# Performance work log

Measured on AMD Instinct MI355X. Metric: run time of the kernel, lower is better.

Reference implementation:

```python
import jax, jax.numpy as jnp
import numpy as np

D_MODEL, H, D_FF = 1024, 16, 4096
D_K = D_MODEL // H
EPS = 1e-5


def _layernorm(x, alpha, bias):
    # faithful to source: unbiased std (ddof=1), eps added to std (not var)
    mean = jnp.mean(x, axis=-1, keepdims=True)
    std = jnp.std(x, axis=-1, keepdims=True, ddof=1)
    return alpha * (x - mean) / (std + EPS) + bias


def setup_inputs() -> dict:
    key = jax.random.key(0)
    ks = jax.random.split(key, 12)
    B, S = 2, 2048
    s = 1.0 / np.sqrt(D_MODEL)
    inp = {
        "x": jax.random.normal(ks[0], (B, S, D_MODEL), dtype=jnp.float32),
        "mask": jnp.ones((B, 1, 1, S), dtype=jnp.int32),
        "wq": jax.random.normal(ks[1], (D_MODEL, D_MODEL), dtype=jnp.float32) * s,
        "wk": jax.random.normal(ks[2], (D_MODEL, D_MODEL), dtype=jnp.float32) * s,
        "wv": jax.random.normal(ks[3], (D_MODEL, D_MODEL), dtype=jnp.float32) * s,
        "wo": jax.random.normal(ks[4], (D_MODEL, D_MODEL), dtype=jnp.float32) * s,
        "w1": jax.random.normal(ks[5], (D_MODEL, D_FF), dtype=jnp.float32) * s,
        "b1": jnp.zeros((D_FF,), dtype=jnp.float32),
        "w2": jax.random.normal(ks[6], (D_FF, D_MODEL), dtype=jnp.float32) * (1.0 / np.sqrt(D_FF)),
        "b2": jnp.zeros((D_MODEL,), dtype=jnp.float32),
        "alpha1": jnp.ones((1,), dtype=jnp.float32),
        "bias1": jnp.zeros((1,), dtype=jnp.float32),
        "alpha2": jnp.ones((1,), dtype=jnp.float32),
        "bias2": jnp.zeros((1,), dtype=jnp.float32),
    }
    return inp


def reference(x, mask, wq, wk, wv, wo, w1, b1, w2, b2, alpha1, bias1, alpha2, bias2):
    B, S, _ = x.shape

    # --- sublayer 1: pre-norm self-attention + residual ---
    xn = _layernorm(x, alpha1, bias1)
    q = (xn @ wq).reshape(B, S, H, D_K).transpose(0, 2, 1, 3)  # [B,H,S,Dk]
    k = (xn @ wk).reshape(B, S, H, D_K).transpose(0, 2, 1, 3)
    v = (xn @ wv).reshape(B, S, H, D_K).transpose(0, 2, 1, 3)

    scores = jnp.einsum("bhqd,bhkd->bhqk", q, k) / np.sqrt(D_K)  # [B,H,S,S]
    scores = jnp.where(mask == 0, jnp.float32(-1e9), scores)
    attn = jax.nn.softmax(scores, axis=-1)
    ctx = jnp.einsum("bhqk,bhkd->bhqd", attn, v)
    ctx = ctx.transpose(0, 2, 1, 3).reshape(B, S, D_MODEL)
    x = x + ctx @ wo

    # --- sublayer 2: pre-norm FFN + residual ---
    xn = _layernorm(x, alpha2, bias2)
    h = jax.nn.relu(xn @ w1 + b1)
    x = x + h @ w2 + b2
    return x
```

## Files before the change

kernel.cpp:

```cpp
#include <hip/hip_runtime.h>
#include <hip/hip_bf16.h>

typedef __attribute__((ext_vector_type(8))) short bf16x8;
typedef __attribute__((ext_vector_type(4))) short short4v;
typedef __attribute__((ext_vector_type(4))) float floatx4;

#define MFMA16(A, B, C) __builtin_amdgcn_mfma_f32_16x16x32_bf16((A), (B), (C), 0, 0, 0)

__device__ inline short bf16bits(float f) {
  __hip_bfloat16 h = __float2bfloat16(f);
  return *reinterpret_cast<short*>(&h);
}
__device__ inline unsigned cvtpk(float lo, float hi) {
  unsigned r;
  asm("v_cvt_pk_bf16_f32 %0, %1, %2" : "=v"(r) : "v"(lo), "v"(hi));
  return r;
}
typedef __attribute__((address_space(3))) char lds_char;
typedef __attribute__((address_space(1))) const char glob_char;
__device__ inline void gll16(const void* g, void* l) {
  __builtin_amdgcn_global_load_lds((glob_char*)g, (lds_char*)l, 16, 0, 0);
}

__global__ __launch_bounds__(256) void ln_qkvtrans_kernel(
    const float* __restrict__ x, __hip_bfloat16* __restrict__ y,
    const float* __restrict__ alpha_p, const float* __restrict__ bias_p,
    const float* __restrict__ wq, const float* __restrict__ wk,
    const float* __restrict__ wv, __hip_bfloat16* __restrict__ wqkvT) {
  __shared__ __align__(16) __hip_bfloat16 tile[64][72];
  const int bid = blockIdx.x;
  const int t = threadIdx.x;
  if (bid < 4096) {
    __shared__ float sred[8];
    const float* xr = x + (long)bid * 1024;
    float v[4];
#pragma unroll
    for (int i = 0; i < 4; i++) v[i] = xr[t * 4 + i];
    float sum = 0.f, sq = 0.f;
#pragma unroll
    for (int i = 0; i < 4; i++) { sum += v[i]; sq += v[i] * v[i]; }
#pragma unroll
    for (int off = 32; off; off >>= 1) {
      sum += __shfl_down(sum, off);
      sq += __shfl_down(sq, off);
    }
    if ((t & 63) == 0) { sred[(t >> 6) * 2] = sum; sred[(t >> 6) * 2 + 1] = sq; }
    __syncthreads();
    sum = sred[0] + sred[2] + sred[4] + sred[6];
    sq = sred[1] + sred[3] + sred[5] + sred[7];
    const float mean = sum * (1.f / 1024.f);
    float var = (sq - 1024.f * mean * mean) * (1.f / 1023.f);
    var = fmaxf(var, 0.f);
    const float denom = sqrtf(var) + 1e-5f;
    const float sc = alpha_p[0] / denom;
    const float beta = bias_p[0];
    __hip_bfloat16* yr = y + (long)bid * 1024;
#pragma unroll
    for (int i = 0; i < 4; i++) yr[t * 4 + i] = __float2bfloat16((v[i] - mean) * sc + beta);
  } else {
    const int tt = bid - 4096;
    const int which = tt >> 8;
    const float* src = which == 0 ? wq : (which == 1 ? wk : wv);
    __hip_bfloat16* dst = wqkvT + (size_t)which * 1024 * 1024;
    const long r0 = (long)((tt >> 4) & 15) * 64, c0 = (long)(tt & 15) * 64;
    for (int i = t; i < 1024; i += 256) {
      int r = i >> 4, c4 = (i & 15) * 4;
      float4 f = *(const float4*)&src[(r0 + r) * 1024 + c0 + c4];
      short4v s;
      s[0] = bf16bits(f.x); s[1] = bf16bits(f.y);
      s[2] = bf16bits(f.z); s[3] = bf16bits(f.w);
      *(short4v*)&tile[r][c4] = s;
    }
    __syncthreads();
    for (int i = t; i < 512; i += 256) {
      int c = i >> 3, r8 = (i & 7) * 8;
      bf16x8 sv;
#pragma unroll
      for (int j = 0; j < 8; j++) sv[j] = *reinterpret_cast<const short*>(&tile[r8 + j][c]);
      *(bf16x8*)&dst[(c0 + c) * 1024 + r0 + r8] = sv;
    }
  }
}

__global__ __launch_bounds__(256) void prep_kernel(
    const __hip_bfloat16* __restrict__ qkv, __hip_bfloat16* __restrict__ vt,
    const float* __restrict__ wo, __hip_bfloat16* __restrict__ woT,
    const int* __restrict__ mask, float* __restrict__ addm,
    int* __restrict__ flags) {
  __shared__ __align__(16) __hip_bfloat16 tile[64][72];
  __shared__ int ok[4];
  const int bid = blockIdx.x;
  if (bid < 1024) {
    const int bh = bid >> 5, b = bh >> 4, h = bh & 15;
    const long s0 = (long)(bid & 31) * 64;
    const __hip_bfloat16* src = qkv + ((long)b * 2048 + s0) * 3072 + 2048 + h * 64;
    for (int i = threadIdx.x; i < 512; i += 256) {
      int s = i >> 3, d8 = (i & 7) * 8;
      *(uint4*)&tile[s][d8] = *(const uint4*)&src[(long)s * 3072 + d8];
    }
    __syncthreads();
    __hip_bfloat16* dstb = vt + (long)bh * 64 * 2048 + s0;
    for (int i = threadIdx.x; i < 512; i += 256) {
      int d = i >> 3, s8 = (i & 7) * 8;
      bf16x8 sv;
#pragma unroll
      for (int j = 0; j < 8; j++) sv[j] = *reinterpret_cast<const short*>(&tile[s8 + j][d]);
      *(bf16x8*)&dstb[(long)d * 2048 + s8] = sv;
    }
  } else if (bid < 1280) {
    const int t = bid - 1024;
    const long r0 = (long)(t >> 4) * 64, c0 = (long)(t & 15) * 64;
    for (int i = threadIdx.x; i < 1024; i += 256) {
      int r = i >> 4, c4 = (i & 15) * 4;
      float4 f = *(const float4*)&wo[(r0 + r) * 1024 + c0 + c4];
      short4v s;
      s[0] = bf16bits(f.x); s[1] = bf16bits(f.y);
      s[2] = bf16bits(f.z); s[3] = bf16bits(f.w);
      *(short4v*)&tile[r][c4] = s;
    }
    __syncthreads();
    for (int i = threadIdx.x; i < 512; i += 256) {
      int c = i >> 3, r8 = (i & 7) * 8;
      bf16x8 sv;
#pragma unroll
      for (int j = 0; j < 8; j++) sv[j] = *reinterpret_cast<const short*>(&tile[r8 + j][c]);
      *(bf16x8*)&woT[(c0 + c) * 1024 + r0 + r8] = sv;
    }
  } else {
    const int i = (bid - 1280) * 256 + threadIdx.x;
    const int mv = mask[i];
    addm[i] = mv ? 0.f : -1e30f;
    const unsigned long long bal = __ballot(mv != 0);
    if ((threadIdx.x & 63) == 0) ok[threadIdx.x >> 6] = (bal == ~0ull) ? 1 : 0;
    __syncthreads();
    if (threadIdx.x == 0) flags[bid - 1280] = ok[0] & ok[1] & ok[2] & ok[3];
  }
}

__global__ __launch_bounds__(256) void wtrans_kernel(
    const float* __restrict__ w1c, const float* __restrict__ w2c,
    __hip_bfloat16* __restrict__ w1Th, __hip_bfloat16* __restrict__ w2Th) {
  __shared__ __align__(16) __hip_bfloat16 tile[64][72];
  const int bid = blockIdx.x;
  const float* src;
  __hip_bfloat16* dst;
  int R, ldS;
  long r0, c0;
  if (bid < 512) {
    src = w1c; dst = w1Th; R = 1024; ldS = 4096;
    r0 = (long)(bid >> 5) * 64; c0 = (long)(bid & 31) * 64;
  } else {
    const int t = bid - 512;
    src = w2c; dst = w2Th; R = 2048; ldS = 1024;
    r0 = (long)(t >> 4) * 64; c0 = (long)(t & 15) * 64;
  }
  for (int i = threadIdx.x; i < 1024; i += 256) {
    int r = i >> 4, c4 = (i & 15) * 4;
    float4 f = *(const float4*)&src[(r0 + r) * ldS + c0 + c4];
    short4v s;
    s[0] = bf16bits(f.x); s[1] = bf16bits(f.y);
    s[2] = bf16bits(f.z); s[3] = bf16bits(f.w);
    *(short4v*)&tile[r][c4] = s;
  }
  __syncthreads();
  for (int i = threadIdx.x; i < 512; i += 256) {
    int c = i >> 3, r8 = (i & 7) * 8;
    bf16x8 sv;
#pragma unroll
    for (int j = 0; j < 8; j++) sv[j] = *reinterpret_cast<const short*>(&tile[r8 + j][c]);
    *(bf16x8*)&dst[(c0 + c) * R + r0 + r8] = sv;
  }
}

__global__ __launch_bounds__(256) void bias_add_kernel(
    const float* __restrict__ x1, const float* __restrict__ b2,
    float* __restrict__ out) {
  const int i = (blockIdx.x * 256 + threadIdx.x) * 4;
  float4 v = *(const float4*)&x1[i];
  const float4 bb = *(const float4*)&b2[i & 1023];
  v.x += bb.x; v.y += bb.y; v.z += bb.z; v.w += bb.w;
  *(float4*)&out[i] = v;
}

__global__ __launch_bounds__(256) void ln_kernel(
    const float* __restrict__ x, __hip_bfloat16* __restrict__ y,
    const float* __restrict__ alpha_p, const float* __restrict__ bias_p) {
  __shared__ float sred[8];
  const long row = blockIdx.x;
  const int t = threadIdx.x;
  const float* xr = x + row * 1024;
  float v[4];
#pragma unroll
  for (int i = 0; i < 4; i++) v[i] = xr[t * 4 + i];
  float sum = 0.f, sq = 0.f;
#pragma unroll
  for (int i = 0; i < 4; i++) { sum += v[i]; sq += v[i] * v[i]; }
#pragma unroll
  for (int off = 32; off; off >>= 1) {
    sum += __shfl_down(sum, off);
    sq += __shfl_down(sq, off);
  }
  if ((t & 63) == 0) { sred[(t >> 6) * 2] = sum; sred[(t >> 6) * 2 + 1] = sq; }
  __syncthreads();
  sum = sred[0] + sred[2] + sred[4] + sred[6];
  sq = sred[1] + sred[3] + sred[5] + sred[7];
  const float mean = sum * (1.f / 1024.f);
  float var = (sq - 1024.f * mean * mean) * (1.f / 1023.f);
  var = fmaxf(var, 0.f);
  const float denom = sqrtf(var) + 1e-5f;
  const float sc = alpha_p[0] / denom;
  const float beta = bias_p[0];
  __hip_bfloat16* yr = y + row * 1024;
#pragma unroll
  for (int i = 0; i < 4; i++) yr[t * 4 + i] = __float2bfloat16((v[i] - mean) * sc + beta);
}

template <int EPI>
__global__ __launch_bounds__(256) void gemm_bt_kernel(
    const __hip_bfloat16* __restrict__ A, const __hip_bfloat16* __restrict__ Bt,
    void* __restrict__ Cv, const float* __restrict__ bias,
    const float* __restrict__ res, int M, int N, int K) {
  __shared__ __align__(16) __hip_bfloat16 lA[2][128 * 32];
  __shared__ __align__(16) __hip_bfloat16 lB[2][128 * 32];
  const int tid = threadIdx.x;
  const int wave = tid >> 6, lane = tid & 63;
  const int quad = lane >> 4, l16 = lane & 15;
  const int wm = wave >> 1, wn = wave & 1;

  const int gx = gridDim.x;
  const int nwg = gx * gridDim.y;
  int bid = blockIdx.y * gx + blockIdx.x;
  bid = (bid & 7) * (nwg >> 3) + (bid >> 3);
  const long m0 = (long)(bid / gx) * 128;
  const long n0 = (long)(bid % gx) * 128;

  const int rA0 = tid >> 2, cA0 = (tid & 3) * 8;
  const int rA1 = (tid + 256) >> 2, cA1 = ((tid + 256) & 3) * 8;

  floatx4 acc[4][4];
#pragma unroll
  for (int i = 0; i < 4; i++)
#pragma unroll
    for (int j = 0; j < 4; j++) acc[i][j] = (floatx4){0.f, 0.f, 0.f, 0.f};

  const __hip_bfloat16* Ab = A + m0 * K;
  const __hip_bfloat16* Bb = Bt + n0 * K;

  gll16(&Ab[(long)rA0 * K + cA0], &lA[0][wave * 512]);
  gll16(&Ab[(long)rA1 * K + cA1], &lA[0][2048 + wave * 512]);
  gll16(&Bb[(long)rA0 * K + cA0], &lB[0][wave * 512]);
  gll16(&Bb[(long)rA1 * K + cA1], &lB[0][2048 + wave * 512]);

  int cur = 0;
  for (int k0 = 0; k0 < K; k0 += 32) {
    __syncthreads();
    if (k0 + 32 < K) {
      const int nxt = cur ^ 1;
      gll16(&Ab[(long)rA0 * K + k0 + 32 + cA0], &lA[nxt][wave * 512]);
      gll16(&Ab[(long)rA1 * K + k0 + 32 + cA1], &lA[nxt][2048 + wave * 512]);
      gll16(&Bb[(long)rA0 * K + k0 + 32 + cA0], &lB[nxt][wave * 512]);
      gll16(&Bb[(long)rA1 * K + k0 + 32 + cA1], &lB[nxt][2048 + wave * 512]);
    }
    bf16x8 af[4], bfr[4];
#pragma unroll
    for (int mi = 0; mi < 4; mi++)
      af[mi] = *(const bf16x8*)&lA[cur][(wm * 64 + mi * 16 + l16) * 32 + quad * 8];
#pragma unroll
    for (int ni = 0; ni < 4; ni++)
      bfr[ni] = *(const bf16x8*)&lB[cur][(wn * 64 + ni * 16 + l16) * 32 + quad * 8];
#pragma unroll
    for (int mi = 0; mi < 4; mi++)
#pragma unroll
      for (int ni = 0; ni < 4; ni++)
        acc[mi][ni] = MFMA16(af[mi], bfr[ni], acc[mi][ni]);
    cur ^= 1;
  }

#pragma unroll
  for (int mi = 0; mi < 4; mi++) {
#pragma unroll
    for (int ni = 0; ni < 4; ni++) {
#pragma unroll
      for (int r = 0; r < 4; r++) {
        const long row = m0 + wm * 64 + mi * 16 + quad * 4 + r;
        const long col = n0 + wn * 64 + ni * 16 + l16;
        const long idx = row * N + col;
        float v = acc[mi][ni][r];
        if (EPI == 0) {
          ((__hip_bfloat16*)Cv)[idx] = __float2bfloat16(v);
        } else if (EPI == 1) {
          ((float*)Cv)[idx] = v + res[idx];
        } else if (EPI == 2) {
          v += bias[col];
          ((__hip_bfloat16*)Cv)[idx] = __float2bfloat16(fmaxf(v, 0.f));
        } else if (EPI == 3) {
          float* Cf = (float*)Cv;
          Cf[idx] = Cf[idx] + v;
        }
      }
    }
  }
}

template <int EPI>
__global__ __launch_bounds__(256) void gemm_bt_k64_kernel(
    const __hip_bfloat16* __restrict__ A, const __hip_bfloat16* __restrict__ Bt,
    void* __restrict__ Cv, const float* __restrict__ bias,
    const float* __restrict__ res, int M, int N, int K) {
  __shared__ __align__(16) __hip_bfloat16 lA[2][128 * 64];
  __shared__ __align__(16) __hip_bfloat16 lB[2][128 * 64];
  const int tid = threadIdx.x;
  const int wave = tid >> 6, lane = tid & 63;
  const int quad = lane >> 4, l16 = lane & 15;
  const int wm = wave >> 1, wn = wave & 1;

  const int gx = gridDim.x;
  const int nwg = gx * gridDim.y;
  int bid = blockIdx.y * gx + blockIdx.x;
  bid = (bid & 7) * (nwg >> 3) + (bid >> 3);
  const long m0 = (long)(bid / gx) * 128;
  const long n0 = (long)(bid % gx) * 128;

  const int srow = lane >> 3;
  const int cg = (lane & 7) ^ srow;

  floatx4 acc[4][4];
#pragma unroll
  for (int i = 0; i < 4; i++)
#pragma unroll
    for (int j = 0; j < 4; j++) acc[i][j] = (floatx4){0.f, 0.f, 0.f, 0.f};

  const __hip_bfloat16* Ab = A + m0 * K;
  const __hip_bfloat16* Bb = Bt + n0 * K;

#pragma unroll
  for (int j = 0; j < 4; ++j) {
    const int c = wave + j * 4;
    gll16(&Ab[(long)(c * 8 + srow) * K + cg * 8], &lA[0][c * 512]);
    gll16(&Bb[(long)(c * 8 + srow) * K + cg * 8], &lB[0][c * 512]);
  }

  int cur = 0;
  for (int k0 = 0; k0 < K; k0 += 64) {
    __syncthreads();
    if (k0 + 64 < K) {
      const int nxt = cur ^ 1;
#pragma unroll
      for (int j = 0; j < 4; ++j) {
        const int c = wave + j * 4;
        gll16(&Ab[(long)(c * 8 + srow) * K + k0 + 64 + cg * 8], &lA[nxt][c * 512]);
        gll16(&Bb[(long)(c * 8 + srow) * K + k0 + 64 + cg * 8], &lB[nxt][c * 512]);
      }
    }
#pragma unroll
    for (int ks = 0; ks < 2; ++ks) {
      bf16x8 af[4], bfr[4];
#pragma unroll
      for (int mi = 0; mi < 4; mi++) {
        const int row = wm * 64 + mi * 16 + l16;
        af[mi] = *(const bf16x8*)&lA[cur][row * 64 +
                                          (((ks * 4 + quad) ^ (l16 & 7)) * 8)];
      }
#pragma unroll
      for (int ni = 0; ni < 4; ni++) {
        const int row = wn * 64 + ni * 16 + l16;
        bfr[ni] = *(const bf16x8*)&lB[cur][row * 64 +
                                           (((ks * 4 + quad) ^ (l16 & 7)) * 8)];
      }
#pragma unroll
      for (int mi = 0; mi < 4; mi++)
#pragma unroll
        for (int ni = 0; ni < 4; ni++)
          acc[mi][ni] = MFMA16(af[mi], bfr[ni], acc[mi][ni]);
    }
    cur ^= 1;
  }

#pragma unroll
  for (int mi = 0; mi < 4; mi++) {
#pragma unroll
    for (int ni = 0; ni < 4; ni++) {
#pragma unroll
      for (int r = 0; r < 4; r++) {
        const long row = m0 + wm * 64 + mi * 16 + quad * 4 + r;
        const long col = n0 + wn * 64 + ni * 16 + l16;
        const long idx = row * N + col;
        float v = acc[mi][ni][r];
        if (EPI == 0) {
          ((__hip_bfloat16*)Cv)[idx] = __float2bfloat16(v);
        } else if (EPI == 1) {
          ((float*)Cv)[idx] = v + res[idx];
        } else if (EPI == 2) {
          v += bias[col];
          ((__hip_bfloat16*)Cv)[idx] = __float2bfloat16(fmaxf(v, 0.f));
        } else if (EPI == 3) {
          float* Cf = (float*)Cv;
          Cf[idx] = Cf[idx] + v;
        }
      }
    }
  }
}

template <int EPI>
__global__ __launch_bounds__(256) void gemm64_bt_kernel(
    const __hip_bfloat16* __restrict__ A, const __hip_bfloat16* __restrict__ Bt,
    void* __restrict__ Cv, const float* __restrict__ bias,
    const float* __restrict__ res, int M, int N, int K) {
  __shared__ __align__(16) __hip_bfloat16 lA[2][128 * 64];
  __shared__ __align__(16) __hip_bfloat16 lB[2][64 * 64];
  const int tid = threadIdx.x;
  const int wave = tid >> 6, lane = tid & 63;
  const int quad = lane >> 4, l16 = lane & 15;
  const int wm = wave >> 1, wn = wave & 1;

  const int gx = gridDim.x;
  const int nwg = gx * gridDim.y;
  int bid = blockIdx.y * gx + blockIdx.x;
  bid = (bid & 7) * (nwg >> 3) + (bid >> 3);
  const long m0 = (long)(bid / gx) * 128;
  const long n0 = (long)(bid % gx) * 64;

  const int srow = lane >> 3;
  const int cg = (lane & 7) ^ srow;

  floatx4 acc[4][2];
#pragma unroll
  for (int i = 0; i < 4; i++)
#pragma unroll
    for (int j = 0; j < 2; j++) acc[i][j] = (floatx4){0.f, 0.f, 0.f, 0.f};

  const __hip_bfloat16* Ab = A + m0 * K;
  const __hip_bfloat16* Bb = Bt + n0 * K;

#pragma unroll
  for (int j = 0; j < 4; ++j) {
    const int c = wave + j * 4;
    gll16(&Ab[(long)(c * 8 + srow) * K + cg * 8], &lA[0][c * 512]);
  }
#pragma unroll
  for (int j = 0; j < 2; ++j) {
    const int c = wave + j * 4;
    gll16(&Bb[(long)(c * 8 + srow) * K + cg * 8], &lB[0][c * 512]);
  }

  int cur = 0;
  for (int k0 = 0; k0 < K; k0 += 64) {
    __syncthreads();
    if (k0 + 64 < K) {
      const int nxt = cur ^ 1;
#pragma unroll
      for (int j = 0; j < 4; ++j) {
        const int c = wave + j * 4;
        gll16(&Ab[(long)(c * 8 + srow) * K + k0 + 64 + cg * 8], &lA[nxt][c * 512]);
      }
#pragma unroll
      for (int j = 0; j < 2; ++j) {
        const int c = wave + j * 4;
        gll16(&Bb[(long)(c * 8 + srow) * K + k0 + 64 + cg * 8], &lB[nxt][c * 512]);
      }
    }
#pragma unroll
    for (int ks = 0; ks < 2; ++ks) {
      bf16x8 af[4], bfr[2];
#pragma unroll
      for (int mi = 0; mi < 4; mi++) {
        const int row = wm * 64 + mi * 16 + l16;
        af[mi] = *(const bf16x8*)&lA[cur][row * 64 +
                                          (((ks * 4 + quad) ^ (l16 & 7)) * 8)];
      }
#pragma unroll
      for (int ni = 0; ni < 2; ni++) {
        const int row = wn * 32 + ni * 16 + l16;
        bfr[ni] = *(const bf16x8*)&lB[cur][row * 64 +
                                           (((ks * 4 + quad) ^ (l16 & 7)) * 8)];
      }
#pragma unroll
      for (int mi = 0; mi < 4; mi++)
#pragma unroll
        for (int ni = 0; ni < 2; ni++)
          acc[mi][ni] = MFMA16(af[mi], bfr[ni], acc[mi][ni]);
    }
    cur ^= 1;
  }

#pragma unroll
  for (int mi = 0; mi < 4; mi++) {
#pragma unroll
    for (int ni = 0; ni < 2; ni++) {
#pragma unroll
      for (int r = 0; r < 4; r++) {
        const long row = m0 + wm * 64 + mi * 16 + quad * 4 + r;
        const long col = n0 + wn * 32 + ni * 16 + l16;
        const long idx = row * N + col;
        float v = acc[mi][ni][r];
        if (EPI == 1) {
          ((float*)Cv)[idx] = v + res[idx];
        } else if (EPI == 3) {
          float* Cf = (float*)Cv;
          Cf[idx] = Cf[idx] + v;
        }
      }
    }
  }
}

__global__ __launch_bounds__(256) void attn_kernel(
    const __hip_bfloat16* __restrict__ qkv, const __hip_bfloat16* __restrict__ vt,
    const float* __restrict__ addm, const int* __restrict__ flags,
    __hip_bfloat16* __restrict__ ctx) {
  __shared__ __align__(16) __hip_bfloat16 lK[2][64 * 64];
  __shared__ __align__(16) __hip_bfloat16 lV[2][64 * 64];
  __shared__ __align__(16) __hip_bfloat16 lP[4][16 * 64];
  const int tid = threadIdx.x, wave = tid >> 6, lane = tid & 63;
  const int quad = lane >> 4, l16 = lane & 15;
  const int bh = blockIdx.y, b = bh >> 4, h = bh & 15;
  const int q0 = blockIdx.x * 64 + wave * 16;
  const float cs = 0.18033688011112042f;
  const float inv_cs = 5.545177444479562f;

  const __hip_bfloat16* kb = qkv + (long)b * 2048 * 3072 + 1024 + h * 64;
  const __hip_bfloat16* vb = vt + (long)bh * 64 * 2048;
  const float* am = addm + b * 2048;

  int fm = 1;
#pragma unroll
  for (int i = 0; i < 8; ++i) fm &= flags[b * 8 + i];
  const bool fast = (fm != 0);

  const long qoff = ((long)b * 2048 + q0 + l16) * 3072 + h * 64;
  const bf16x8 bq0 = *(const bf16x8*)&qkv[qoff + quad * 8];
  const bf16x8 bq1 = *(const bf16x8*)&qkv[qoff + 32 + quad * 8];

  const int srow = lane >> 3;
  const int cslot = lane & 7;
  const int cg = cslot ^ srow;
  const int rbase = wave * 16 + srow;

  char* const pbase = (char*)&lP[wave][0];
  const int prow = l16 * 128;
  const int pswz = l16 & 7;

  floatx4 o[4];
#pragma unroll
  for (int mi = 0; mi < 4; mi++) o[mi] = (floatx4){0.f, 0.f, 0.f, 0.f};
  float mrow = 10.0f, lrow = 0.f;

#pragma unroll
  for (int j = 0; j < 2; ++j) {
    const int rloc = rbase + j * 8;
    gll16(kb + (long)rloc * 3072 + cg * 8, &lK[0][(wave * 16 + j * 8) * 64]);
    gll16(vb + (long)rloc * 2048 + cg * 8, &lV[0][(wave * 16 + j * 8) * 64]);
  }

  int cur = 0;
  for (int t = 0; t < 32; ++t) {
    __syncthreads();
    if (t + 1 < 32) {
      const int nxt = cur ^ 1;
#pragma unroll
      for (int j = 0; j < 2; ++j) {
        const int rloc = rbase + j * 8;
        gll16(kb + (long)((t + 1) * 64 + rloc) * 3072 + cg * 8,
              &lK[nxt][(wave * 16 + j * 8) * 64]);
        gll16(vb + (long)rloc * 2048 + (t + 1) * 64 + cg * 8,
              &lV[nxt][(wave * 16 + j * 8) * 64]);
      }
    }
    const __hip_bfloat16* lKc = lK[cur];
    const __hip_bfloat16* lVc = lV[cur];

    floatx4 c[4];
    __builtin_amdgcn_s_setprio(1);
#pragma unroll
    for (int g = 0; g < 4; ++g) {
      const bf16x8 a0 =
          *(const bf16x8*)&lKc[(g * 16 + l16) * 64 + ((quad) ^ (l16 & 7)) * 8];
      const bf16x8 a1 =
          *(const bf16x8*)&lKc[(g * 16 + l16) * 64 + ((4 + quad) ^ (l16 & 7)) * 8];
      floatx4 cc = {0.f, 0.f, 0.f, 0.f};
      cc = MFMA16(a0, bq0, cc);
      cc = MFMA16(a1, bq1, cc);
      c[g] = cc;
    }
    __builtin_amdgcn_s_setprio(0);

    if (!fast) {
#pragma unroll
      for (int g = 0; g < 4; ++g) {
        const float4 a4 = *(const float4*)&am[t * 64 + g * 16 + quad * 4];
        c[g][0] = fmaf(a4.x, inv_cs, c[g][0]);
        c[g][1] = fmaf(a4.y, inv_cs, c[g][1]);
        c[g][2] = fmaf(a4.z, inv_cs, c[g][2]);
        c[g][3] = fmaf(a4.w, inv_cs, c[g][3]);
      }
    }

    const float mneg = -mrow;
    float p[4][4];
#pragma unroll
    for (int g = 0; g < 4; ++g)
#pragma unroll
      for (int r = 0; r < 4; ++r)
        p[g][r] = __builtin_amdgcn_exp2f(fmaf(c[g][r], cs, mneg));

#pragma unroll
    for (int g = 0; g < 4; ++g) {
      uint2 w2;
      w2.x = cvtpk(p[g][0], p[g][1]);
      w2.y = cvtpk(p[g][2], p[g][3]);
      const int slot16 = (g * 2 + (quad >> 1)) ^ pswz;
      *(uint2*)(pbase + prow + (slot16 << 4) + ((quad & 1) << 3)) = w2;
    }

    const float m0 = fmaxf(fmaxf(c[0][0], c[0][1]), c[0][2]);
    const float m1 = fmaxf(fmaxf(c[0][3], c[1][0]), c[1][1]);
    const float m2 = fmaxf(fmaxf(c[1][2], c[1][3]), c[2][0]);
    const float m3 = fmaxf(fmaxf(c[2][1], c[2][2]), c[2][3]);
    const float m4 = fmaxf(fmaxf(c[3][0], c[3][1]), c[3][2]);
    float tm = fmaxf(fmaxf(fmaxf(m0, m1), fmaxf(m2, m3)), fmaxf(m4, c[3][3]));
    tm = fmaxf(tm, __shfl_xor(tm, 16));
    tm = fmaxf(tm, __shfl_xor(tm, 32));
    const float tms = tm * cs;

    const float s0 = (p[0][0] + p[0][1]) + (p[0][2] + p[0][3]);
    const float s1 = (p[1][0] + p[1][1]) + (p[1][2] + p[1][3]);
    const float s2 = (p[2][0] + p[2][1]) + (p[2][2] + p[2][3]);
    const float s3 = (p[3][0] + p[3][1]) + (p[3][2] + p[3][3]);
    float rs = (s0 + s1) + (s2 + s3);
    rs += __shfl_xor(rs, 16);
    rs += __shfl_xor(rs, 32);

#pragma unroll
    for (int ss = 0; ss < 2; ++ss) {
      const bf16x8 bp = *(const bf16x8*)(pbase + prow +
                                         ((((ss << 2) + quad) ^ pswz) << 4));
      __builtin_amdgcn_s_setprio(1);
#pragma unroll
      for (int mi = 0; mi < 4; ++mi) {
        const bf16x8 av = *(const bf16x8*)&lVc[(mi * 16 + l16) * 64 +
                                               ((ss * 4 + quad) ^ (l16 & 7)) * 8];
        o[mi] = MFMA16(av, bp, o[mi]);
      }
      __builtin_amdgcn_s_setprio(0);
    }

    lrow += rs;
    if (__any(tms > mrow + 8.f)) {
      const float mnew = fmaxf(mrow, tms);
      const float alpha = __builtin_amdgcn_exp2f(mrow - mnew);
      mrow = mnew;
      lrow *= alpha;
#pragma unroll
      for (int mi = 0; mi < 4; mi++) o[mi] *= alpha;
    }
    cur ^= 1;
  }

  const float inv_l = 1.f / lrow;
  const long cb = ((long)b * 2048 + q0 + l16) * 1024 + h * 64;
#pragma unroll
  for (int mi = 0; mi < 4; mi++) {
    uint2 st;
    st.x = cvtpk(o[mi][0] * inv_l, o[mi][1] * inv_l);
    st.y = cvtpk(o[mi][2] * inv_l, o[mi][3] * inv_l);
    *(uint2*)&ctx[cb + mi * 16 + quad * 4] = st;
  }
}

extern "C" void kernel_launch(void* const* d_in, const int* in_sizes, int n_in,
                              void* d_out, int out_size, void* d_ws, size_t ws_size,
                              hipStream_t stream) {
  const float* x = (const float*)d_in[0];
  const int* mask = (const int*)d_in[1];
  const float* wq = (const float*)d_in[2];
  const float* wk = (const float*)d_in[3];
  const float* wv = (const float*)d_in[4];
  const float* wo = (const float*)d_in[5];
  const float* w1 = (const float*)d_in[6];
  const float* b1 = (const float*)d_in[7];
  const float* w2 = (const float*)d_in[8];
  const float* b2 = (const float*)d_in[9];
  const float* alpha1 = (const float*)d_in[10];
  const float* bias1 = (const float*)d_in[11];
  const float* alpha2 = (const float*)d_in[12];
  const float* bias2 = (const float*)d_in[13];

  char* ws = (char*)d_ws;
  char* dob = (char*)d_out;
  const size_t MiB = 1048576;
  __hip_bfloat16* qkv   = (__hip_bfloat16*)(ws + 0);
  __hip_bfloat16* wqkvT = (__hip_bfloat16*)(ws + 24 * MiB);
  __hip_bfloat16* vtb   = (__hip_bfloat16*)(ws + 24 * MiB);
  float*          x1    = (float*)(ws + 0);
  __hip_bfloat16* hc    = (__hip_bfloat16*)(ws + 16 * MiB);
  __hip_bfloat16* xn    = (__hip_bfloat16*)d_out;
  __hip_bfloat16* ctxb  = (__hip_bfloat16*)d_out;
  __hip_bfloat16* xn2   = (__hip_bfloat16*)d_out;
  __hip_bfloat16* woT   = (__hip_bfloat16*)(dob + 8 * MiB);
  __hip_bfloat16* w1Th  = (__hip_bfloat16*)(dob + 8 * MiB);
  __hip_bfloat16* w2Th  = (__hip_bfloat16*)(dob + 12 * MiB);
  float*          addm  = (float*)(dob + 12 * MiB);
  int*            flags = (int*)(dob + 12 * MiB + 16 * 1024);

  const dim3 b256(256);
  ln_qkvtrans_kernel<<<4864, b256, 0, stream>>>(x, xn, alpha1, bias1,
                                                wq, wk, wv, wqkvT);
  gemm_bt_kernel<0><<<dim3(24, 32), b256, 0, stream>>>(xn, wqkvT, qkv, nullptr, nullptr,
                                                       4096, 3072, 1024);
  prep_kernel<<<1296, b256, 0, stream>>>(qkv, vtb, wo, woT, mask, addm, flags);
  attn_kernel<<<dim3(32, 32), b256, 0, stream>>>(qkv, vtb, addm, flags, ctxb);
  gemm64_bt_kernel<1><<<dim3(16, 32), b256, 0, stream>>>(ctxb, woT, x1, nullptr, x,
                                                         4096, 1024, 1024);
  ln_kernel<<<4096, b256, 0, stream>>>(x1, xn2, alpha2, bias2);
  for (int c = 0; c < 2; ++c) {
    wtrans_kernel<<<1024, b256, 0, stream>>>(w1 + c * 2048,
                                             w2 + (size_t)c * 2048 * 1024,
                                             w1Th, w2Th);
    gemm_bt_k64_kernel<2><<<dim3(16, 32), b256, 0, stream>>>(xn2, w1Th, hc,
                                                             b1 + c * 2048, nullptr,
                                                             4096, 2048, 1024);
    gemm64_bt_kernel<3><<<dim3(16, 32), b256, 0, stream>>>(hc, w2Th, x1, nullptr,
                                                           nullptr, 4096, 1024, 2048);
  }
  bias_add_kernel<<<4096, b256, 0, stream>>>(x1, b2, (float*)d_out);
}
```

Measured before the change: 384.4 us.

## Process two query fragments per wave in attention, switch QKV GEMM to k64 variant

Each attention wave now handles 32 query rows as two 16-row fragments, so each K/V tile loaded into LDS serves twice as many queries. The grid is halved to match. This cuts K/V global traffic and barrier overhead per query, at the cost of more registers, a larger P buffer in LDS, and fewer blocks (512) to fill the GPU. Separately, the QKV projection now uses the gemm_bt_k64 kernel variant instead of gemm_bt.

```diff
diff --git a/kernel.cpp b/kernel.cpp
--- a/kernel.cpp
+++ b/kernel.cpp
@@ -511,11 +511,11 @@
     __hip_bfloat16* __restrict__ ctx) {
   __shared__ __align__(16) __hip_bfloat16 lK[2][64 * 64];
   __shared__ __align__(16) __hip_bfloat16 lV[2][64 * 64];
-  __shared__ __align__(16) __hip_bfloat16 lP[4][16 * 64];
+  __shared__ __align__(16) __hip_bfloat16 lP[4][32 * 64];
   const int tid = threadIdx.x, wave = tid >> 6, lane = tid & 63;
   const int quad = lane >> 4, l16 = lane & 15;
   const int bh = blockIdx.y, b = bh >> 4, h = bh & 15;
-  const int q0 = blockIdx.x * 64 + wave * 16;
+  const int q0 = blockIdx.x * 128 + wave * 32;
   const float cs = 0.18033688011112042f;
   const float inv_cs = 5.545177444479562f;
 
@@ -528,9 +528,13 @@
   for (int i = 0; i < 8; ++i) fm &= flags[b * 8 + i];
   const bool fast = (fm != 0);
 
-  const long qoff = ((long)b * 2048 + q0 + l16) * 3072 + h * 64;
-  const bf16x8 bq0 = *(const bf16x8*)&qkv[qoff + quad * 8];
-  const bf16x8 bq1 = *(const bf16x8*)&qkv[qoff + 32 + quad * 8];
+  bf16x8 bq[2][2];
+#pragma unroll
+  for (int f = 0; f < 2; ++f) {
+    const long qoff = ((long)b * 2048 + q0 + f * 16 + l16) * 3072 + h * 64;
+    bq[f][0] = *(const bf16x8*)&qkv[qoff + quad * 8];
+    bq[f][1] = *(const bf16x8*)&qkv[qoff + 32 + quad * 8];
+  }
 
   const int srow = lane >> 3;
   const int cslot = lane & 7;
@@ -538,13 +542,14 @@
   const int rbase = wave * 16 + srow;
 
   char* const pbase = (char*)&lP[wave][0];
-  const int prow = l16 * 128;
   const int pswz = l16 & 7;
 
-  floatx4 o[4];
-#pragma unroll
-  for (int mi = 0; mi < 4; mi++) o[mi] = (floatx4){0.f, 0.f, 0.f, 0.f};
-  float mrow = 10.0f, lrow = 0.f;
+  floatx4 o[2][4];
+#pragma unroll
+  for (int f = 0; f < 2; ++f)
+#pragma unroll
+    for (int mi = 0; mi < 4; mi++) o[f][mi] = (floatx4){0.f, 0.f, 0.f, 0.f};
+  float mrow[2] = {10.0f, 10.0f}, lrow[2] = {0.f, 0.f};
 
 #pragma unroll
   for (int j = 0; j < 2; ++j) {
@@ -570,101 +575,117 @@
     const __hip_bfloat16* lKc = lK[cur];
     const __hip_bfloat16* lVc = lV[cur];
 
-    floatx4 c[4];
-    __builtin_amdgcn_s_setprio(1);
-#pragma unroll
-    for (int g = 0; g < 4; ++g) {
-      const bf16x8 a0 =
-          *(const bf16x8*)&lKc[(g * 16 + l16) * 64 + ((quad) ^ (l16 & 7)) * 8];
-      const bf16x8 a1 =
-          *(const bf16x8*)&lKc[(g * 16 + l16) * 64 + ((4 + quad) ^ (l16 & 7)) * 8];
-      floatx4 cc = {0.f, 0.f, 0.f, 0.f};
-      cc = MFMA16(a0, bq0, cc);
-      cc = MFMA16(a1, bq1, cc);
-      c[g] = cc;
-    }
-    __builtin_amdgcn_s_setprio(0);
-
-    if (!fast) {
+    float tms[2], rs[2];
+#pragma unroll
+    for (int f = 0; f < 2; ++f) {
+      floatx4 c[4];
+      __builtin_amdgcn_s_setprio(1);
 #pragma unroll
       for (int g = 0; g < 4; ++g) {
-        const float4 a4 = *(const float4*)&am[t * 64 + g * 16 + quad * 4];
-        c[g][0] = fmaf(a4.x, inv_cs, c[g][0]);
-        c[g][1] = fmaf(a4.y, inv_cs, c[g][1]);
-        c[g][2] = fmaf(a4.z, inv_cs, c[g][2]);
-        c[g][3] = fmaf(a4.w, inv_cs, c[g][3]);
-      }
-    }
-
-    const float mneg = -mrow;
-    float p[4][4];
-#pragma unroll
-    for (int g = 0; g < 4; ++g)
-#pragma unroll
-      for (int r = 0; r < 4; ++r)
-        p[g][r] = __builtin_amdgcn_exp2f(fmaf(c[g][r], cs, mneg));
-
-#pragma unroll
-    for (int g = 0; g < 4; ++g) {
-      uint2 w2;
-      w2.x = cvtpk(p[g][0], p[g][1]);
-      w2.y = cvtpk(p[g][2], p[g][3]);
-      const int slot16 = (g * 2 + (quad >> 1)) ^ pswz;
-      *(uint2*)(pbase + prow + (slot16 << 4) + ((quad & 1) << 3)) = w2;
-    }
-
-    const float m0 = fmaxf(fmaxf(c[0][0], c[0][1]), c[0][2]);
-    const float m1 = fmaxf(fmaxf(c[0][3], c[1][0]), c[1][1]);
-    const float m2 = fmaxf(fmaxf(c[1][2], c[1][3]), c[2][0]);
-    const float m3 = fmaxf(fmaxf(c[2][1], c[2][2]), c[2][3]);
-    const float m4 = fmaxf(fmaxf(c[3][0], c[3][1]), c[3][2]);
-    float tm = fmaxf(fmaxf(fmaxf(m0, m1), fmaxf(m2, m3)), fmaxf(m4, c[3][3]));
-    tm = fmaxf(tm, __shfl_xor(tm, 16));
-    tm = fmaxf(tm, __shfl_xor(tm, 32));
-    const float tms = tm * cs;
-
-    const float s0 = (p[0][0] + p[0][1]) + (p[0][2] + p[0][3]);
-    const float s1 = (p[1][0] + p[1][1]) + (p[1][2] + p[1][3]);
-    const float s2 = (p[2][0] + p[2][1]) + (p[2][2] + p[2][3]);
-    const float s3 = (p[3][0] + p[3][1]) + (p[3][2] + p[3][3]);
-    float rs = (s0 + s1) + (s2 + s3);
-    rs += __shfl_xor(rs, 16);
-    rs += __shfl_xor(rs, 32);
-
-#pragma unroll
-    for (int ss = 0; ss < 2; ++ss) {
-      const bf16x8 bp = *(const bf16x8*)(pbase + prow +
-                                         ((((ss << 2) + quad) ^ pswz) << 4));
-      __builtin_amdgcn_s_setprio(1);
-#pragma unroll
-      for (int mi = 0; mi < 4; ++mi) {
-        const bf16x8 av = *(const bf16x8*)&lVc[(mi * 16 + l16) * 64 +
-                                               ((ss * 4 + quad) ^ (l16 & 7)) * 8];
-        o[mi] = MFMA16(av, bp, o[mi]);
+        const bf16x8 a0 =
+            *(const bf16x8*)&lKc[(g * 16 + l16) * 64 + ((quad) ^ (l16 & 7)) * 8];
+        const bf16x8 a1 =
+            *(const bf16x8*)&lKc[(g * 16 + l16) * 64 + ((4 + quad) ^ (l16 & 7)) * 8];
+        floatx4 cc = {0.f, 0.f, 0.f, 0.f};
+        cc = MFMA16(a0, bq[f][0], cc);
+        cc = MFMA16(a1, bq[f][1], cc);
+        c[g] = cc;
       }
       __builtin_amdgcn_s_setprio(0);
-    }
-
-    lrow += rs;
-    if (__any(tms > mrow + 8.f)) {
-      const float mnew = fmaxf(mrow, tms);
-      const float alpha = __builtin_amdgcn_exp2f(mrow - mnew);
-      mrow = mnew;
-      lrow *= alpha;
-#pragma unroll
-      for (int mi = 0; mi < 4; mi++) o[mi] *= alpha;
+
+      if (!fast) {
+#pragma unroll
+        for (int g = 0; g < 4; ++g) {
+          const float4 a4 = *(const float4*)&am[t * 64 + g * 16 + quad * 4];
+          c[g][0] = fmaf(a4.x, inv_cs, c[g][0]);
+          c[g][1] = fmaf(a4.y, inv_cs, c[g][1]);
+          c[g][2] = fmaf(a4.z, inv_cs, c[g][2]);
+          c[g][3] = fmaf(a4.w, inv_cs, c[g][3]);
+        }
+      }
+
+      const float mneg = -mrow[f];
+      float p[4][4];
+#pragma unroll
+      for (int g = 0; g < 4; ++g)
+#pragma unroll
+        for (int r = 0; r < 4; ++r)
+          p[g][r] = __builtin_amdgcn_exp2f(fmaf(c[g][r], cs, mneg));
+
+      const int prow = (f * 16 + l16) * 128;
+#pragma unroll
+      for (int g = 0; g < 4; ++g) {
+        uint2 w2;
+        w2.x = cvtpk(p[g][0], p[g][1]);
+        w2.y = cvtpk(p[g][2], p[g][3]);
+        const int slot16 = (g * 2 + (quad >> 1)) ^ pswz;
+        *(uint2*)(pbase + prow + (slot16 << 4) + ((quad & 1) << 3)) = w2;
+      }
+
+      const float m0 = fmaxf(fmaxf(c[0][0], c[0][1]), c[0][2]);
+      const float m1 = fmaxf(fmaxf(c[0][3], c[1][0]), c[1][1]);
+      const float m2 = fmaxf(fmaxf(c[1][2], c[1][3]), c[2][0]);
+      const float m3 = fmaxf(fmaxf(c[2][1], c[2][2]), c[2][3]);
+      const float m4 = fmaxf(fmaxf(c[3][0], c[3][1]), c[3][2]);
+      float tm = fmaxf(fmaxf(fmaxf(m0, m1), fmaxf(m2, m3)), fmaxf(m4, c[3][3]));
+      tm = fmaxf(tm, __shfl_xor(tm, 16));
+      tm = fmaxf(tm, __shfl_xor(tm, 32));
+      tms[f] = tm * cs;
+
+      const float s0 = (p[0][0] + p[0][1]) + (p[0][2] + p[0][3]);
+      const float s1 = (p[1][0] + p[1][1]) + (p[1][2] + p[1][3]);
+      const float s2 = (p[2][0] + p[2][1]) + (p[2][2] + p[2][3]);
+      const float s3 = (p[3][0] + p[3][1]) + (p[3][2] + p[3][3]);
+      float r = (s0 + s1) + (s2 + s3);
+      r += __shfl_xor(r, 16);
+      r += __shfl_xor(r, 32);
+      rs[f] = r;
+    }
+
+#pragma unroll
+    for (int f = 0; f < 2; ++f) {
+      const int prow = (f * 16 + l16) * 128;
+#pragma unroll
+      for (int ss = 0; ss < 2; ++ss) {
+        const bf16x8 bp = *(const bf16x8*)(pbase + prow +
+                                           ((((ss << 2) + quad) ^ pswz) << 4));
+        __builtin_amdgcn_s_setprio(1);
+#pragma unroll
+        for (int mi = 0; mi < 4; ++mi) {
+          const bf16x8 av = *(const bf16x8*)&lVc[(mi * 16 + l16) * 64 +
+                                                 ((ss * 4 + quad) ^ (l16 & 7)) * 8];
+          o[f][mi] = MFMA16(av, bp, o[f][mi]);
+        }
+        __builtin_amdgcn_s_setprio(0);
+      }
+    }
+
+#pragma unroll
+    for (int f = 0; f < 2; ++f) {
+      lrow[f] += rs[f];
+      if (__any(tms[f] > mrow[f] + 8.f)) {
+        const float mnew = fmaxf(mrow[f], tms[f]);
+        const float alpha = __builtin_amdgcn_exp2f(mrow[f] - mnew);
+        mrow[f] = mnew;
+        lrow[f] *= alpha;
+#pragma unroll
+        for (int mi = 0; mi < 4; mi++) o[f][mi] *= alpha;
+      }
     }
     cur ^= 1;
   }
 
-  const float inv_l = 1.f / lrow;
-  const long cb = ((long)b * 2048 + q0 + l16) * 1024 + h * 64;
-#pragma unroll
-  for (int mi = 0; mi < 4; mi++) {
-    uint2 st;
-    st.x = cvtpk(o[mi][0] * inv_l, o[mi][1] * inv_l);
-    st.y = cvtpk(o[mi][2] * inv_l, o[mi][3] * inv_l);
-    *(uint2*)&ctx[cb + mi * 16 + quad * 4] = st;
+#pragma unroll
+  for (int f = 0; f < 2; ++f) {
+    const float inv_l = 1.f / lrow[f];
+    const long cb = ((long)b * 2048 + q0 + f * 16 + l16) * 1024 + h * 64;
+#pragma unroll
+    for (int mi = 0; mi < 4; mi++) {
+      uint2 st;
+      st.x = cvtpk(o[f][mi][0] * inv_l, o[f][mi][1] * inv_l);
+      st.y = cvtpk(o[f][mi][2] * inv_l, o[f][mi][3] * inv_l);
+      *(uint2*)&ctx[cb + mi * 16 + quad * 4] = st;
+    }
   }
 }
 
@@ -706,10 +727,11 @@
   const dim3 b256(256);
   ln_qkvtrans_kernel<<<4864, b256, 0, stream>>>(x, xn, alpha1, bias1,
                                                 wq, wk, wv, wqkvT);
-  gemm_bt_kernel<0><<<dim3(24, 32), b256, 0, stream>>>(xn, wqkvT, qkv, nullptr, nullptr,
-                                                       4096, 3072, 1024);
+  gemm_bt_k64_kernel<0><<<dim3(24, 32), b256, 0, stream>>>(xn, wqkvT, qkv,
+                                                           nullptr, nullptr,
+                                                           4096, 3072, 1024);
   prep_kernel<<<1296, b256, 0, stream>>>(qkv, vtb, wo, woT, mask, addm, flags);
-  attn_kernel<<<dim3(32, 32), b256, 0, stream>>>(qkv, vtb, addm, flags, ctxb);
+  attn_kernel<<<dim3(16, 32), b256, 0, stream>>>(qkv, vtb, addm, flags, ctxb);
   gemm64_bt_kernel<1><<<dim3(16, 32), b256, 0, stream>>>(ctxb, woT, x1, nullptr, x,
                                                          4096, 1024, 1024);
   ln_kernel<<<4096, b256, 0, stream>>>(x1, xn2, alpha2, bias2);
```

After: 395.7 us. 2.9% more time.
